# Performance work log

Hardware: AMD Instinct MI355X
Metric: run time of the kernel (lower is better)

The kernel has to match this reference:

```python
import jax, jax.numpy as jnp
import numpy as np

B, L, D = 8, 4096, 512
KS = (3, 5, 7)
EPS = 1e-5
W_SCALE = 0.02  # tame torch.randn-style init for numerical sanity


def layernorm(x, g, b):
    mu = jnp.mean(x, axis=-1, keepdims=True)
    var = jnp.var(x, axis=-1, keepdims=True)
    return (x - mu) * jax.lax.rsqrt(var + EPS) * g + b


def masked_conv(x1, chain, W, b):
    # x1: (B, C, L); W: (O, C, K); chain: (B, L) int32
    K = W.shape[2]
    pad_l = (K - 1) // 2
    pad_r = (K - 1) - pad_l
    xp = jnp.pad(x1, ((0, 0), (0, 0), (pad_l, pad_r)))
    ip = jnp.pad(chain, ((0, 0), (pad_l, pad_r)))  # pad id = 0
    Lx = x1.shape[2]
    # center tap of each window is the position's own chain id (odd K, center == pad_l)
    out = b[None, :, None]
    for k in range(K):  # small static loop over taps
        xs = xp[:, :, k:k + Lx]                      # (B, C, L)
        mk = (ip[:, k:k + Lx] == chain)              # (B, L) bool
        out = out + jnp.einsum('bcl,oc->bol', xs * mk[:, None, :], W[:, :, k])
    return out


def setup_inputs() -> dict:
    key = jax.random.key(0)
    ks = jax.random.split(key, 16)
    inp = {
        'x': jax.random.normal(ks[0], (B, L, D), dtype=jnp.float32),
        'chain': jnp.sort(jax.random.randint(ks[1], (B, L), 0, 8), axis=-1).astype(jnp.int32),
    }
    for i, (name, K) in enumerate(zip(('W3', 'W5', 'W7'), KS)):
        inp[name] = jax.random.normal(ks[2 + i], (D, D, K), dtype=jnp.float32) * W_SCALE
        inp['b' + name[1:]] = jax.random.normal(ks[5 + i], (D,), dtype=jnp.float32) * W_SCALE
    inp['mlp_w1'] = jax.random.normal(ks[8], (D, 4 * D), dtype=jnp.float32) * W_SCALE
    inp['mlp_b1'] = jnp.zeros((4 * D,), dtype=jnp.float32)
    inp['mlp_w2'] = jax.random.normal(ks[9], (4 * D, D), dtype=jnp.float32) * W_SCALE
    inp['mlp_b2'] = jnp.zeros((D,), dtype=jnp.float32)
    inp['ln1_g'] = jnp.ones((D,), dtype=jnp.float32)
    inp['ln1_b'] = jnp.zeros((D,), dtype=jnp.float32)
    inp['ln2_g'] = jnp.ones((D,), dtype=jnp.float32)
    inp['ln2_b'] = jnp.zeros((D,), dtype=jnp.float32)
    return inp


def reference(x, chain, W3, b3, W5, b5, W7, b7,
              mlp_w1, mlp_b1, mlp_w2, mlp_b2,
              ln1_g, ln1_b, ln2_g, ln2_b):
    x1 = jnp.transpose(x, (0, 2, 1))  # (B, C, L)
    for W, b in ((W3, b3), (W5, b5), (W7, b7)):
        x1 = masked_conv(x1, chain, W, b)
    h = layernorm(x + jnp.transpose(x1, (0, 2, 1)), ln1_g, ln1_b)
    mlp = jax.nn.gelu(h @ mlp_w1 + mlp_b1) @ mlp_w2 + mlp_b2
    return layernorm(h + mlp, ln2_g, ln2_b)
```

## Files before the change

### kernel.cpp

```cpp
#include <hip/hip_runtime.h>
#include <math.h>

#define BB 8
#define LL 4096
#define DD 512
#define PTOT (BB*LL)
#define HID  2048

typedef __attribute__((ext_vector_type(8))) short short8;
typedef __attribute__((ext_vector_type(4))) float f32x4;

typedef __attribute__((address_space(1))) const unsigned int gconst_u32;
typedef __attribute__((address_space(3))) unsigned int lds_u32;

__device__ __forceinline__ void gload16(const void* g, void* l) {
    __builtin_amdgcn_global_load_lds((gconst_u32*)g, (lds_u32*)l, 16, 0, 0);
}

__device__ __forceinline__ unsigned short f2bf(float f) {
    union { float f; unsigned int u; } v; v.f = f;
    unsigned int r = v.u + 0x7fffu + ((v.u >> 16) & 1u);
    return (unsigned short)(r >> 16);
}
__device__ __forceinline__ float bf2f(unsigned short h) {
    union { unsigned int u; float f; } v; v.u = ((unsigned int)h) << 16;
    return v.f;
}
__device__ __forceinline__ float gelu_fast(float x) {
    float x2 = x * x;
    float t  = x * fmaf(0.044715f, x2, 1.0f);
    float e  = __builtin_amdgcn_exp2f(-2.3021143f * t);
    return x * __builtin_amdgcn_rcpf(1.0f + e);
}

__global__ __launch_bounds__(256) void convert_x(const float* __restrict__ x,
                                                 unsigned short* __restrict__ xb,
                                                 unsigned short* __restrict__ zp) {
    int tid = blockIdx.x * 256 + threadIdx.x;
    if (blockIdx.x == 0 && threadIdx.x < 128) zp[threadIdx.x] = 0;
    float4 v = ((const float4*)x)[tid];
    uint2 o;
    o.x = (unsigned int)f2bf(v.x) | ((unsigned int)f2bf(v.y) << 16);
    o.y = (unsigned int)f2bf(v.z) | ((unsigned int)f2bf(v.w) << 16);
    ((uint2*)xb)[tid] = o;
}

__global__ __launch_bounds__(256) void trans_wconv(const float* __restrict__ W,
                                                   unsigned short* __restrict__ Wt, int K) {
    int tid = blockIdx.x * 256 + threadIdx.x;
    if (tid >= DD * DD * K) return;
    int o  = tid / (K * DD);
    int kc = tid - o * K * DD;
    int k  = kc >> 9;
    int c  = kc & (DD - 1);
    Wt[tid] = f2bf(W[(o * DD + c) * K + k]);
}

__global__ __launch_bounds__(256) void trans_w1(const float* __restrict__ W,
                                                unsigned short* __restrict__ Wt) {
    int tid = blockIdx.x * 256 + threadIdx.x;
    int n = tid >> 9;
    int c = tid & (DD - 1);
    Wt[tid] = f2bf(W[c * HID + n]);
}

__global__ __launch_bounds__(256) void trans_w2(const float* __restrict__ W,
                                                unsigned short* __restrict__ Wt) {
    int tid = blockIdx.x * 256 + threadIdx.x;
    int n = tid >> 11;
    int h = tid & (HID - 1);
    Wt[tid] = f2bf(W[h * DD + n]);
}

__global__ __launch_bounds__(256) void make_srcp(const int* __restrict__ chain,
                                                 int* __restrict__ srcp, int K) {
    int tid = blockIdx.x * 256 + threadIdx.x;
    if (tid >= PTOT * K) return;
    int p = tid / K;
    int k = tid - p * K;
    int b = p >> 12;
    int l = p & (LL - 1);
    int pad = (K - 1) >> 1;
    int l2 = l + k - pad;
    bool ok = (l2 >= 0) && (l2 < LL) && (chain[b * LL + l2] == chain[b * LL + l]);
    srcp[tid] = ok ? (p + k - pad) : -1;
}

template <int TAPS, int EPI>
__global__ __launch_bounds__(256, 3) void mfma_gemm(
        const unsigned short* __restrict__ A, int lda,
        const int* __restrict__ srcp,
        const unsigned short* __restrict__ Bt, int ldb,
        const float* __restrict__ bias,
        void* __restrict__ Yv, int ldc, int Kspan,
        const unsigned short* __restrict__ zp) {
    __shared__ alignas(16) unsigned short As[128 * 64];
    __shared__ alignas(16) unsigned short Bs[128 * 64];

    int t = threadIdx.x;
    int p0 = blockIdx.x * 128;
    int o0 = blockIdx.y * 128;
    int w = t >> 6, lane = t & 63;
    int wr = w & 1, wc = w >> 1;
    int lm = lane & 15, q = lane >> 4;

    int lrow8 = lane >> 3;
    int qq = (lane & 7) ^ lrow8;

    unsigned short* a_dst = As + w * 2048;
    unsigned short* b_dst = Bs + w * 2048;

    int boff[4];
#pragma unroll
    for (int j = 0; j < 4; j++)
        boff[j] = (o0 + w * 32 + j * 8 + lrow8) * ldb + qq * 8;

    f32x4 acc[4][4];
#pragma unroll
    for (int mi = 0; mi < 4; mi++)
#pragma unroll
        for (int nj = 0; nj < 4; nj++) acc[mi][nj] = (f32x4){0.f, 0.f, 0.f, 0.f};

    const int NT = TAPS ? TAPS : 1;
    for (int tap = 0; tap < NT; ++tap) {
        int aoff[4];
#pragma unroll
        for (int i = 0; i < 4; i++) {
            int r = p0 + w * 32 + i * 8 + lrow8;
            int sp = TAPS ? srcp[r * TAPS + tap] : r;
            aoff[i] = (sp >= 0) ? (sp * lda + qq * 8) : -1;
        }
        const int span = TAPS ? DD : Kspan;
        const int kb0  = TAPS ? tap * DD : 0;
        for (int kc = 0; kc < span; kc += 64) {
#pragma unroll
            for (int i = 0; i < 4; i++) {
                const unsigned short* g = (aoff[i] >= 0) ? (A + aoff[i] + kc) : zp;
                gload16(g, a_dst + i * 512);
            }
#pragma unroll
            for (int j = 0; j < 4; j++)
                gload16(Bt + boff[j] + kb0 + kc, b_dst + j * 512);
            __syncthreads();

#pragma unroll
            for (int kk = 0; kk < 2; kk++) {
                int sa = ((kk * 4 + q) ^ (lm & 7)) * 8;
                short8 b[4];
#pragma unroll
                for (int nj = 0; nj < 4; nj++)
                    b[nj] = *(const short8*)&Bs[(wc * 64 + nj * 16 + lm) * 64 + sa];
#pragma unroll
                for (int mi = 0; mi < 4; mi++) {
                    short8 a = *(const short8*)&As[(wr * 64 + mi * 16 + lm) * 64 + sa];
#pragma unroll
                    for (int nj = 0; nj < 4; nj++)
                        acc[mi][nj] = __builtin_amdgcn_mfma_f32_16x16x32_bf16(
                            a, b[nj], acc[mi][nj], 0, 0, 0);
                }
            }
            __syncthreads();
        }
    }

#pragma unroll
    for (int mi = 0; mi < 4; mi++) {
#pragma unroll
        for (int nj = 0; nj < 4; nj++) {
            int col = o0 + wc * 64 + nj * 16 + lm;
#pragma unroll
            for (int r = 0; r < 4; r++) {
                int row = p0 + wr * 64 + mi * 16 + q * 4 + r;
                float v = acc[mi][nj][r];
                size_t idx = (size_t)row * ldc + col;
                if (EPI == 0) {
                    ((unsigned short*)Yv)[idx] = f2bf(v + bias[col]);
                } else if (EPI == 1) {
                    ((unsigned short*)Yv)[idx] = f2bf(gelu_fast(v + bias[col]));
                } else if (EPI == 2) {
                    ((float*)Yv)[idx] = v + bias[col];
                } else {
                    ((float*)Yv)[idx] += v;
                }
            }
        }
    }
}

__global__ __launch_bounds__(256) void ln1_kernel(const float* __restrict__ x,
                                                  const unsigned short* __restrict__ conv,
                                                  const float* __restrict__ g,
                                                  const float* __restrict__ beta,
                                                  unsigned short* __restrict__ h) {
    int p = blockIdx.x, t = threadIdx.x;
    size_t base = (size_t)p * DD;
    float v0 = x[base + t] + bf2f(conv[base + t]);
    float v1 = x[base + 256 + t] + bf2f(conv[base + 256 + t]);
    float s = v0 + v1, sq = v0 * v0 + v1 * v1;
#pragma unroll
    for (int off = 32; off > 0; off >>= 1) { s += __shfl_xor(s, off); sq += __shfl_xor(sq, off); }
    __shared__ float red[2][4];
    int wid = t >> 6, lane = t & 63;
    if (lane == 0) { red[0][wid] = s; red[1][wid] = sq; }
    __syncthreads();
    float S = red[0][0] + red[0][1] + red[0][2] + red[0][3];
    float SQ = red[1][0] + red[1][1] + red[1][2] + red[1][3];
    float mu = S * (1.f / DD);
    float var = SQ * (1.f / DD) - mu * mu;
    float rs = rsqrtf(var + 1e-5f);
    h[base + t]       = f2bf((v0 - mu) * rs * g[t] + beta[t]);
    h[base + 256 + t] = f2bf((v1 - mu) * rs * g[256 + t] + beta[256 + t]);
}

__global__ __launch_bounds__(256) void ln2_kernel(const unsigned short* __restrict__ h,
                                                  float* __restrict__ out,
                                                  const float* __restrict__ g,
                                                  const float* __restrict__ beta) {
    int p = blockIdx.x, t = threadIdx.x;
    size_t base = (size_t)p * DD;
    float v0 = bf2f(h[base + t]) + out[base + t];
    float v1 = bf2f(h[base + 256 + t]) + out[base + 256 + t];
    float s = v0 + v1, sq = v0 * v0 + v1 * v1;
#pragma unroll
    for (int off = 32; off > 0; off >>= 1) { s += __shfl_xor(s, off); sq += __shfl_xor(sq, off); }
    __shared__ float red[2][4];
    int wid = t >> 6, lane = t & 63;
    if (lane == 0) { red[0][wid] = s; red[1][wid] = sq; }
    __syncthreads();
    float S = red[0][0] + red[0][1] + red[0][2] + red[0][3];
    float SQ = red[1][0] + red[1][1] + red[1][2] + red[1][3];
    float mu = S * (1.f / DD);
    float var = SQ * (1.f / DD) - mu * mu;
    float rs = rsqrtf(var + 1e-5f);
    out[base + t]       = (v0 - mu) * rs * g[t] + beta[t];
    out[base + 256 + t] = (v1 - mu) * rs * g[256 + t] + beta[256 + t];
}

extern "C" void kernel_launch(void* const* d_in, const int* in_sizes, int n_in,
                              void* d_out, int out_size, void* d_ws, size_t ws_size,
                              hipStream_t stream) {
    const float* x     = (const float*)d_in[0];
    const int*   chain = (const int*)d_in[1];
    const float* W3    = (const float*)d_in[2];
    const float* b3    = (const float*)d_in[3];
    const float* W5    = (const float*)d_in[4];
    const float* b5    = (const float*)d_in[5];
    const float* W7    = (const float*)d_in[6];
    const float* b7    = (const float*)d_in[7];
    const float* w1    = (const float*)d_in[8];
    const float* bm1   = (const float*)d_in[9];
    const float* w2    = (const float*)d_in[10];
    const float* bm2   = (const float*)d_in[11];
    const float* g1    = (const float*)d_in[12];
    const float* be1   = (const float*)d_in[13];
    const float* g2    = (const float*)d_in[14];
    const float* be2   = (const float*)d_in[15];
    float* out = (float*)d_out;

    const size_t ACT = (size_t)PTOT * DD * 2;
    char* ws = (char*)d_ws;
    size_t off = 0;
    unsigned short* Xb   = (unsigned short*)(ws + off); off += ACT;
    unsigned short* buf1 = (unsigned short*)(ws + off); off += ACT;
    unsigned short* buf2 = (unsigned short*)(ws + off); off += ACT;
    unsigned short* w3t  = (unsigned short*)(ws + off); off += (size_t)3 * DD * DD * 2;
    unsigned short* w5t  = (unsigned short*)(ws + off); off += (size_t)5 * DD * DD * 2;
    unsigned short* w7t  = (unsigned short*)(ws + off); off += (size_t)7 * DD * DD * 2;
    unsigned short* w1t  = (unsigned short*)(ws + off); off += (size_t)DD * HID * 2;
    unsigned short* w2t  = (unsigned short*)(ws + off); off += (size_t)DD * HID * 2;
    int* srcp3 = (int*)(ws + off); off += (size_t)PTOT * 3 * 4;
    int* srcp5 = (int*)(ws + off); off += (size_t)PTOT * 5 * 4;
    int* srcp7 = (int*)(ws + off); off += (size_t)PTOT * 7 * 4;
    unsigned short* zp = (unsigned short*)(ws + off); off += 256;
    size_t base_off = off;
    bool full = (ws_size >= base_off + (size_t)PTOT * HID * 2);
    unsigned short* Hb = (unsigned short*)(ws + base_off);

    convert_x<<<PTOT * DD / (256 * 4), 256, 0, stream>>>(x, Xb, zp);
    trans_wconv<<<(DD * DD * 3 + 255) / 256, 256, 0, stream>>>(W3, w3t, 3);
    trans_wconv<<<(DD * DD * 5 + 255) / 256, 256, 0, stream>>>(W5, w5t, 5);
    trans_wconv<<<(DD * DD * 7 + 255) / 256, 256, 0, stream>>>(W7, w7t, 7);
    trans_w1<<<DD * HID / 256, 256, 0, stream>>>(w1, w1t);
    trans_w2<<<DD * HID / 256, 256, 0, stream>>>(w2, w2t);
    make_srcp<<<(PTOT * 3 + 255) / 256, 256, 0, stream>>>(chain, srcp3, 3);
    make_srcp<<<(PTOT * 5 + 255) / 256, 256, 0, stream>>>(chain, srcp5, 5);
    make_srcp<<<(PTOT * 7 + 255) / 256, 256, 0, stream>>>(chain, srcp7, 7);

    dim3 gconv(PTOT / 128, DD / 128);

    mfma_gemm<3, 0><<<gconv, 256, 0, stream>>>(Xb, DD, srcp3, w3t, 3 * DD, b3, buf1, DD, DD, zp);
    mfma_gemm<5, 0><<<gconv, 256, 0, stream>>>(buf1, DD, srcp5, w5t, 5 * DD, b5, buf2, DD, DD, zp);
    mfma_gemm<7, 0><<<gconv, 256, 0, stream>>>(buf2, DD, srcp7, w7t, 7 * DD, b7, buf1, DD, DD, zp);

    ln1_kernel<<<PTOT, 256, 0, stream>>>(x, buf1, g1, be1, buf2);

    if (full) {
        dim3 g1d(PTOT / 128, HID / 128);
        mfma_gemm<0, 1><<<g1d, 256, 0, stream>>>(buf2, DD, nullptr, w1t, DD, bm1,
                                                 Hb, HID, DD, zp);
        mfma_gemm<0, 2><<<gconv, 256, 0, stream>>>(Hb, HID, nullptr, w2t, HID, bm2,
                                                   out, DD, HID, zp);
    } else {
        for (int jc = 0; jc < 4; jc++) {
            mfma_gemm<0, 1><<<gconv, 256, 0, stream>>>(buf2, DD, nullptr,
                                                       w1t + (size_t)jc * DD * DD, DD,
                                                       bm1 + jc * DD, Hb, DD, DD, zp);
            if (jc == 0)
                mfma_gemm<0, 2><<<gconv, 256, 0, stream>>>(Hb, DD, nullptr,
                                                           w2t + jc * DD, HID, bm2,
                                                           out, DD, DD, zp);
            else
                mfma_gemm<0, 3><<<gconv, 256, 0, stream>>>(Hb, DD, nullptr,
                                                           w2t + jc * DD, HID, bm2,
                                                           out, DD, DD, zp);
        }
    }

    ln2_kernel<<<PTOT, 256, 0, stream>>>(buf2, out, g2, be2);
}
```

Baseline: 693.6 us.

## Reuse haloed activation tile across conv taps with per-row bitmask and double-buffered weights

The conv kernels now load one 144-row activation tile (128 rows plus an 8-row halo on each side) per k-chunk and reuse it for every tap, shifting the LDS row index and zeroing masked rows from a per-position 7-bit chain mask. Before, each tap re-gathered its A tile from global memory through a srcp index array. Weight tiles for the next tap are double-buffered in LDS so their loads overlap the current tap's MFMAs. The three srcp index arrays are replaced by a single byte mask, and the plain GEMM is split into its own simpler kernel. LDS use rises to about 50 KB per block, which may limit occupancy, and the halo and swizzle index arithmetic is more complex.

```diff
diff --git a/kernel.cpp b/kernel.cpp
--- a/kernel.cpp
+++ b/kernel.cpp
@@ -34,10 +34,8 @@
 }
 
 __global__ __launch_bounds__(256) void convert_x(const float* __restrict__ x,
-                                                 unsigned short* __restrict__ xb,
-                                                 unsigned short* __restrict__ zp) {
+                                                 unsigned short* __restrict__ xb) {
     int tid = blockIdx.x * 256 + threadIdx.x;
-    if (blockIdx.x == 0 && threadIdx.x < 128) zp[threadIdx.x] = 0;
     float4 v = ((const float4*)x)[tid];
     uint2 o;
     o.x = (unsigned int)f2bf(v.x) | ((unsigned int)f2bf(v.y) << 16);
@@ -72,30 +70,36 @@
     Wt[tid] = f2bf(W[h * DD + n]);
 }
 
-__global__ __launch_bounds__(256) void make_srcp(const int* __restrict__ chain,
-                                                 int* __restrict__ srcp, int K) {
-    int tid = blockIdx.x * 256 + threadIdx.x;
-    if (tid >= PTOT * K) return;
-    int p = tid / K;
-    int k = tid - p * K;
+__global__ __launch_bounds__(256) void make_maskb(const int* __restrict__ chain,
+                                                  unsigned char* __restrict__ mb,
+                                                  unsigned short* __restrict__ zp) {
+    int p = blockIdx.x * 256 + threadIdx.x;
+    if (blockIdx.x == 0 && threadIdx.x < 128) zp[threadIdx.x] = 0;
     int b = p >> 12;
     int l = p & (LL - 1);
-    int pad = (K - 1) >> 1;
-    int l2 = l + k - pad;
-    bool ok = (l2 >= 0) && (l2 < LL) && (chain[b * LL + l2] == chain[b * LL + l]);
-    srcp[tid] = ok ? (p + k - pad) : -1;
-}
-
-template <int TAPS, int EPI>
-__global__ __launch_bounds__(256, 3) void mfma_gemm(
-        const unsigned short* __restrict__ A, int lda,
-        const int* __restrict__ srcp,
-        const unsigned short* __restrict__ Bt, int ldb,
+    int c0 = chain[p];
+    unsigned m = 0;
+#pragma unroll
+    for (int d = -3; d <= 3; d++) {
+        int l2 = l + d;
+        bool ok = (l2 >= 0) && (l2 < LL) && (chain[b * LL + l2] == c0);
+        m |= (ok ? 1u : 0u) << (d + 3);
+    }
+    mb[p] = (unsigned char)m;
+}
+
+template <int K>
+__global__ __launch_bounds__(256, 3) void conv_mfma(
+        const unsigned short* __restrict__ A,
+        const unsigned char* __restrict__ maskb,
+        const unsigned short* __restrict__ Bt,
         const float* __restrict__ bias,
-        void* __restrict__ Yv, int ldc, int Kspan,
+        unsigned short* __restrict__ Y,
         const unsigned short* __restrict__ zp) {
-    __shared__ alignas(16) unsigned short As[128 * 64];
-    __shared__ alignas(16) unsigned short Bs[128 * 64];
+    const int PAD = (K - 1) / 2;
+    const int LDB = K * DD;
+    __shared__ alignas(16) unsigned short As[144 * 64];
+    __shared__ alignas(16) unsigned short Bs[2][128 * 64];
 
     int t = threadIdx.x;
     int p0 = blockIdx.x * 128;
@@ -103,17 +107,27 @@
     int w = t >> 6, lane = t & 63;
     int wr = w & 1, wc = w >> 1;
     int lm = lane & 15, q = lane >> 4;
-
     int lrow8 = lane >> 3;
     int qq = (lane & 7) ^ lrow8;
 
-    unsigned short* a_dst = As + w * 2048;
-    unsigned short* b_dst = Bs + w * 2048;
-
-    int boff[4];
+    unsigned int mbits[4];
+#pragma unroll
+    for (int mi = 0; mi < 4; mi++)
+        mbits[mi] = maskb[p0 + wr * 64 + mi * 16 + lm];
+
+    size_t brow[4];
 #pragma unroll
     for (int j = 0; j < 4; j++)
-        boff[j] = (o0 + w * 32 + j * 8 + lrow8) * ldb + qq * 8;
+        brow[j] = (size_t)(o0 + w * 32 + j * 8 + lrow8) * LDB + qq * 8;
+
+    const unsigned short* agp[5];
+    int nch = (w < 2) ? 5 : 4;
+#pragma unroll
+    for (int i = 0; i < 5; i++) {
+        int c = (i < 4) ? (w + 4 * i) : (16 + w);
+        int gr = p0 - 8 + c * 8 + lrow8;
+        agp[i] = (gr >= 0 && gr < PTOT) ? (A + (size_t)gr * DD + qq * 8) : zp;
+    }
 
     f32x4 acc[4][4];
 #pragma unroll
@@ -121,38 +135,47 @@
 #pragma unroll
         for (int nj = 0; nj < 4; nj++) acc[mi][nj] = (f32x4){0.f, 0.f, 0.f, 0.f};
 
-    const int NT = TAPS ? TAPS : 1;
-    for (int tap = 0; tap < NT; ++tap) {
-        int aoff[4];
-#pragma unroll
-        for (int i = 0; i < 4; i++) {
-            int r = p0 + w * 32 + i * 8 + lrow8;
-            int sp = TAPS ? srcp[r * TAPS + tap] : r;
-            aoff[i] = (sp >= 0) ? (sp * lda + qq * 8) : -1;
-        }
-        const int span = TAPS ? DD : Kspan;
-        const int kb0  = TAPS ? tap * DD : 0;
-        for (int kc = 0; kc < span; kc += 64) {
-#pragma unroll
-            for (int i = 0; i < 4; i++) {
-                const unsigned short* g = (aoff[i] >= 0) ? (A + aoff[i] + kc) : zp;
-                gload16(g, a_dst + i * 512);
+    for (int kc = 0; kc < DD; kc += 64) {
+        for (int i = 0; i < nch; i++) {
+            int c = (i < 4) ? (w + 4 * i) : (16 + w);
+            const unsigned short* g = agp[i];
+            gload16((g == zp) ? g : (g + kc), As + c * 512);
+        }
+#pragma unroll
+        for (int j = 0; j < 4; j++)
+            gload16(Bt + brow[j] + kc, Bs[0] + w * 2048 + j * 512);
+        __syncthreads();
+
+        for (int tap = 0; tap < K; tap++) {
+            int cur = tap & 1;
+            if (tap + 1 < K) {
+#pragma unroll
+                for (int j = 0; j < 4; j++)
+                    gload16(Bt + brow[j] + (size_t)(tap + 1) * DD + kc,
+                            Bs[cur ^ 1] + w * 2048 + j * 512);
             }
-#pragma unroll
-            for (int j = 0; j < 4; j++)
-                gload16(Bt + boff[j] + kb0 + kc, b_dst + j * 512);
-            __syncthreads();
+            int d  = tap - PAD;
+            int mb = tap - PAD + 3;
+            bool keep[4];
+#pragma unroll
+            for (int mi = 0; mi < 4; mi++) keep[mi] = (mbits[mi] >> mb) & 1;
+            int rm = (lm + d) & 7;
 
 #pragma unroll
             for (int kk = 0; kk < 2; kk++) {
-                int sa = ((kk * 4 + q) ^ (lm & 7)) * 8;
+                int slot = kk * 4 + q;
+                int sab = (slot ^ (lm & 7)) * 8;
+                int saa = (slot ^ rm) * 8;
                 short8 b[4];
 #pragma unroll
                 for (int nj = 0; nj < 4; nj++)
-                    b[nj] = *(const short8*)&Bs[(wc * 64 + nj * 16 + lm) * 64 + sa];
+                    b[nj] = *(const short8*)&Bs[cur][(wc * 64 + nj * 16 + lm) * 64 + sab];
 #pragma unroll
                 for (int mi = 0; mi < 4; mi++) {
-                    short8 a = *(const short8*)&As[(wr * 64 + mi * 16 + lm) * 64 + sa];
+                    int hr = 8 + wr * 64 + mi * 16 + lm + d;
+                    short8 a = *(const short8*)&As[hr * 64 + saa];
+                    short8 zero = {};
+                    a = keep[mi] ? a : zero;
 #pragma unroll
                     for (int nj = 0; nj < 4; nj++)
                         acc[mi][nj] = __builtin_amdgcn_mfma_f32_16x16x32_bf16(
@@ -171,11 +194,83 @@
 #pragma unroll
             for (int r = 0; r < 4; r++) {
                 int row = p0 + wr * 64 + mi * 16 + q * 4 + r;
+                Y[(size_t)row * DD + col] = f2bf(acc[mi][nj][r] + bias[col]);
+            }
+        }
+    }
+}
+
+template <int EPI>
+__global__ __launch_bounds__(256, 3) void mfma_gemm(
+        const unsigned short* __restrict__ A, int lda,
+        const unsigned short* __restrict__ Bt, int ldb,
+        const float* __restrict__ bias,
+        void* __restrict__ Yv, int ldc, int Kspan) {
+    __shared__ alignas(16) unsigned short As[128 * 64];
+    __shared__ alignas(16) unsigned short Bs[128 * 64];
+
+    int t = threadIdx.x;
+    int p0 = blockIdx.x * 128;
+    int o0 = blockIdx.y * 128;
+    int w = t >> 6, lane = t & 63;
+    int wr = w & 1, wc = w >> 1;
+    int lm = lane & 15, q = lane >> 4;
+    int lrow8 = lane >> 3;
+    int qq = (lane & 7) ^ lrow8;
+
+    unsigned short* a_dst = As + w * 2048;
+    unsigned short* b_dst = Bs + w * 2048;
+
+    int aoff[4], boff[4];
+#pragma unroll
+    for (int i = 0; i < 4; i++) {
+        aoff[i] = (p0 + w * 32 + i * 8 + lrow8) * lda + qq * 8;
+        boff[i] = (o0 + w * 32 + i * 8 + lrow8) * ldb + qq * 8;
+    }
+
+    f32x4 acc[4][4];
+#pragma unroll
+    for (int mi = 0; mi < 4; mi++)
+#pragma unroll
+        for (int nj = 0; nj < 4; nj++) acc[mi][nj] = (f32x4){0.f, 0.f, 0.f, 0.f};
+
+    for (int kc = 0; kc < Kspan; kc += 64) {
+#pragma unroll
+        for (int i = 0; i < 4; i++) {
+            gload16(A + aoff[i] + kc, a_dst + i * 512);
+            gload16(Bt + boff[i] + kc, b_dst + i * 512);
+        }
+        __syncthreads();
+#pragma unroll
+        for (int kk = 0; kk < 2; kk++) {
+            int sa = ((kk * 4 + q) ^ (lm & 7)) * 8;
+            short8 b[4];
+#pragma unroll
+            for (int nj = 0; nj < 4; nj++)
+                b[nj] = *(const short8*)&Bs[(wc * 64 + nj * 16 + lm) * 64 + sa];
+#pragma unroll
+            for (int mi = 0; mi < 4; mi++) {
+                short8 a = *(const short8*)&As[(wr * 64 + mi * 16 + lm) * 64 + sa];
+#pragma unroll
+                for (int nj = 0; nj < 4; nj++)
+                    acc[mi][nj] = __builtin_amdgcn_mfma_f32_16x16x32_bf16(
+                        a, b[nj], acc[mi][nj], 0, 0, 0);
+            }
+        }
+        __syncthreads();
+    }
+
+#pragma unroll
+    for (int mi = 0; mi < 4; mi++) {
+#pragma unroll
+        for (int nj = 0; nj < 4; nj++) {
+            int col = o0 + wc * 64 + nj * 16 + lm;
+#pragma unroll
+            for (int r = 0; r < 4; r++) {
+                int row = p0 + wr * 64 + mi * 16 + q * 4 + r;
                 float v = acc[mi][nj][r];
                 size_t idx = (size_t)row * ldc + col;
-                if (EPI == 0) {
-                    ((unsigned short*)Yv)[idx] = f2bf(v + bias[col]);
-                } else if (EPI == 1) {
+                if (EPI == 1) {
                     ((unsigned short*)Yv)[idx] = f2bf(gelu_fast(v + bias[col]));
                 } else if (EPI == 2) {
                     ((float*)Yv)[idx] = v + bias[col];
@@ -268,51 +363,42 @@
     unsigned short* w7t  = (unsigned short*)(ws + off); off += (size_t)7 * DD * DD * 2;
     unsigned short* w1t  = (unsigned short*)(ws + off); off += (size_t)DD * HID * 2;
     unsigned short* w2t  = (unsigned short*)(ws + off); off += (size_t)DD * HID * 2;
-    int* srcp3 = (int*)(ws + off); off += (size_t)PTOT * 3 * 4;
-    int* srcp5 = (int*)(ws + off); off += (size_t)PTOT * 5 * 4;
-    int* srcp7 = (int*)(ws + off); off += (size_t)PTOT * 7 * 4;
-    unsigned short* zp = (unsigned short*)(ws + off); off += 256;
+    unsigned char* maskb = (unsigned char*)(ws + off); off += PTOT;
+    unsigned short* zp   = (unsigned short*)(ws + off); off += 256;
     size_t base_off = off;
     bool full = (ws_size >= base_off + (size_t)PTOT * HID * 2);
     unsigned short* Hb = (unsigned short*)(ws + base_off);
 
-    convert_x<<<PTOT * DD / (256 * 4), 256, 0, stream>>>(x, Xb, zp);
+    convert_x<<<PTOT * DD / (256 * 4), 256, 0, stream>>>(x, Xb);
     trans_wconv<<<(DD * DD * 3 + 255) / 256, 256, 0, stream>>>(W3, w3t, 3);
     trans_wconv<<<(DD * DD * 5 + 255) / 256, 256, 0, stream>>>(W5, w5t, 5);
     trans_wconv<<<(DD * DD * 7 + 255) / 256, 256, 0, stream>>>(W7, w7t, 7);
     trans_w1<<<DD * HID / 256, 256, 0, stream>>>(w1, w1t);
     trans_w2<<<DD * HID / 256, 256, 0, stream>>>(w2, w2t);
-    make_srcp<<<(PTOT * 3 + 255) / 256, 256, 0, stream>>>(chain, srcp3, 3);
-    make_srcp<<<(PTOT * 5 + 255) / 256, 256, 0, stream>>>(chain, srcp5, 5);
-    make_srcp<<<(PTOT * 7 + 255) / 256, 256, 0, stream>>>(chain, srcp7, 7);
+    make_maskb<<<PTOT / 256, 256, 0, stream>>>(chain, maskb, zp);
 
     dim3 gconv(PTOT / 128, DD / 128);
 
-    mfma_gemm<3, 0><<<gconv, 256, 0, stream>>>(Xb, DD, srcp3, w3t, 3 * DD, b3, buf1, DD, DD, zp);
-    mfma_gemm<5, 0><<<gconv, 256, 0, stream>>>(buf1, DD, srcp5, w5t, 5 * DD, b5, buf2, DD, DD, zp);
-    mfma_gemm<7, 0><<<gconv, 256, 0, stream>>>(buf2, DD, srcp7, w7t, 7 * DD, b7, buf1, DD, DD, zp);
+    conv_mfma<3><<<gconv, 256, 0, stream>>>(Xb, maskb, w3t, b3, buf1, zp);
+    conv_mfma<5><<<gconv, 256, 0, stream>>>(buf1, maskb, w5t, b5, buf2, zp);
+    conv_mfma<7><<<gconv, 256, 0, stream>>>(buf2, maskb, w7t, b7, buf1, zp);
 
     ln1_kernel<<<PTOT, 256, 0, stream>>>(x, buf1, g1, be1, buf2);
 
     if (full) {
         dim3 g1d(PTOT / 128, HID / 128);
-        mfma_gemm<0, 1><<<g1d, 256, 0, stream>>>(buf2, DD, nullptr, w1t, DD, bm1,
-                                                 Hb, HID, DD, zp);
-        mfma_gemm<0, 2><<<gconv, 256, 0, stream>>>(Hb, HID, nullptr, w2t, HID, bm2,
-                                                   out, DD, HID, zp);
+        mfma_gemm<1><<<g1d, 256, 0, stream>>>(buf2, DD, w1t, DD, bm1, Hb, HID, DD);
+        mfma_gemm<2><<<gconv, 256, 0, stream>>>(Hb, HID, w2t, HID, bm2, out, DD, HID);
     } else {
         for (int jc = 0; jc < 4; jc++) {
-            mfma_gemm<0, 1><<<gconv, 256, 0, stream>>>(buf2, DD, nullptr,
-                                                       w1t + (size_t)jc * DD * DD, DD,
-                                                       bm1 + jc * DD, Hb, DD, DD, zp);
+            mfma_gemm<1><<<gconv, 256, 0, stream>>>(buf2, DD, w1t + (size_t)jc * DD * DD,
+                                                    DD, bm1 + jc * DD, Hb, DD, DD);
             if (jc == 0)
-                mfma_gemm<0, 2><<<gconv, 256, 0, stream>>>(Hb, DD, nullptr,
-                                                           w2t + jc * DD, HID, bm2,
-                                                           out, DD, DD, zp);
+                mfma_gemm<2><<<gconv, 256, 0, stream>>>(Hb, DD, w2t + jc * DD, HID, bm2,
+                                                        out, DD, DD);
             else
-                mfma_gemm<0, 3><<<gconv, 256, 0, stream>>>(Hb, DD, nullptr,
-                                                           w2t + jc * DD, HID, bm2,
-                                                           out, DD, DD, zp);
+                mfma_gemm<3><<<gconv, 256, 0, stream>>>(Hb, DD, w2t + jc * DD, HID, bm2,
+                                                        out, DD, DD);
         }
     }
 
```

Measured after the change: 708.7 us. 1.02x slower.
